# Performance work log

Hardware: AMD Instinct MI355X
Metric: run time of the kernel (lower is better)

The kernel has to match this reference:

```python
import jax, jax.numpy as jnp
import numpy as np

D_MODEL, H, G = 2048, 32, 8
D_K = D_MODEL // H          # 64
GROUP_SIZE = H // G         # 4
B, S = 2, 2048


def setup_inputs() -> dict:
    key = jax.random.key(0)
    ks = jax.random.split(key, 9)
    sd = 1.0 / np.sqrt(D_MODEL)
    x = jax.random.normal(ks[0], (B, S, D_MODEL), dtype=jnp.float32)
    Wq = jax.random.normal(ks[1], (D_MODEL, D_MODEL), dtype=jnp.float32) * sd
    bq = jax.random.normal(ks[2], (D_MODEL,), dtype=jnp.float32) * 0.01
    Wk = jax.random.normal(ks[3], (D_MODEL, G * D_K), dtype=jnp.float32) * sd
    bk = jax.random.normal(ks[4], (G * D_K,), dtype=jnp.float32) * 0.01
    Wv = jax.random.normal(ks[5], (D_MODEL, G * D_K), dtype=jnp.float32) * sd
    bv = jax.random.normal(ks[6], (G * D_K,), dtype=jnp.float32) * 0.01
    Wo = jax.random.normal(ks[7], (D_MODEL, D_MODEL), dtype=jnp.float32) * sd
    bo = jax.random.normal(ks[8], (D_MODEL,), dtype=jnp.float32) * 0.01
    return {"x": x, "Wq": Wq, "bq": bq, "Wk": Wk, "bk": bk,
            "Wv": Wv, "bv": bv, "Wo": Wo, "bo": bo}


def reference(x, Wq, bq, Wk, bk, Wv, bv, Wo, bo):
    Bsz, Sln, _ = x.shape
    # projections
    Q = (x @ Wq + bq).reshape(Bsz, Sln, H, D_K).transpose(0, 2, 1, 3)   # [B,h,S,dk]
    K = (x @ Wk + bk).reshape(Bsz, Sln, G, D_K).transpose(0, 2, 1, 3)   # [B,g,S,dk]
    V = (x @ Wv + bv).reshape(Bsz, Sln, G, D_K).transpose(0, 2, 1, 3)   # [B,g,S,dk]
    # reshape Q into groups: [B, g, group_size, S, dk]; K/V broadcast over group dim
    Qg = Q.reshape(Bsz, G, GROUP_SIZE, Sln, D_K)
    scores = jnp.einsum('bgmqd,bgkd->bgmqk', Qg, K) / jnp.sqrt(jnp.float32(D_K))
    attn = jax.nn.softmax(scores, axis=-1)                              # [B,g,gs,S,S]
    out = jnp.einsum('bgmqk,bgkd->bgmqd', attn, V)                      # [B,g,gs,S,dk]
    out = out.reshape(Bsz, H, Sln, D_K).transpose(0, 2, 1, 3).reshape(Bsz, Sln, D_MODEL)
    return out @ Wo + bo
```

## Files before the change

kernel.cpp:

```cpp
#include <hip/hip_runtime.h>
#include <stdint.h>

#define DMODEL 2048
#define NHEADS 32
#define NGRP 8
#define DKH 64
#define BATCH 2
#define SEQ 2048
#define MTOT (BATCH*SEQ)

typedef unsigned short u16;
typedef __bf16 bf16x8 __attribute__((ext_vector_type(8)));
typedef float f32x4 __attribute__((ext_vector_type(4)));
typedef _Float16 f16x4 __attribute__((ext_vector_type(4)));
typedef _Float16 f16x8 __attribute__((ext_vector_type(8)));
typedef _Float16 f16x2 __attribute__((ext_vector_type(2)));

#define QSCALE 0.18033688011112042f

__device__ __forceinline__ u16 f2bf(float f){
    uint32_t x = __float_as_uint(f);
    x += 0x7FFFu + ((x >> 16) & 1u);
    return (u16)(x >> 16);
}

__device__ __forceinline__ void gld_lds16(const u16* g, u16* l){
    __builtin_amdgcn_global_load_lds(
        (const __attribute__((address_space(1))) uint32_t*)g,
        (__attribute__((address_space(3))) uint32_t*)l, 16, 0, 0);
}


__global__ void cvt_x_kern(const float* __restrict__ x, u16* __restrict__ xb){
    int i = (blockIdx.x * 256 + threadIdx.x) * 4;
    float4 v = *(const float4*)(x + i);
    uint32_t lo = (uint32_t)f2bf(v.x) | ((uint32_t)f2bf(v.y) << 16);
    uint32_t hi = (uint32_t)f2bf(v.z) | ((uint32_t)f2bf(v.w) << 16);
    *(uint2*)(xb + i) = make_uint2(lo, hi);
}

__global__ void cvt_wT_all(const float* __restrict__ Wq, const float* __restrict__ Wk,
                           const float* __restrict__ Wv, const float* __restrict__ Wo,
                           u16* __restrict__ WqT, u16* __restrict__ WkT,
                           u16* __restrict__ WvT, u16* __restrict__ WoT){
    __shared__ float t[32][33];
    int bx = blockIdx.x;
    const float* W; u16* T; int N; int cx;
    if (bx < 64)      { W = Wq; T = WqT; N = 2048; cx = bx; }
    else if (bx < 80) { W = Wk; T = WkT; N = 512;  cx = bx - 64; }
    else if (bx < 96) { W = Wv; T = WvT; N = 512;  cx = bx - 80; }
    else              { W = Wo; T = WoT; N = 2048; cx = bx - 96; }
    int tx = threadIdx.x & 31, ty = threadIdx.x >> 5;
    int n0 = cx * 32, k0 = blockIdx.y * 32;
#pragma unroll
    for (int i = 0; i < 4; i++)
        t[ty*4+i][tx] = W[(size_t)(k0 + ty*4 + i) * N + n0 + tx];
    __syncthreads();
#pragma unroll
    for (int i = 0; i < 4; i++)
        T[(size_t)(n0 + ty*4 + i) * DMODEL + k0 + tx] = f2bf(t[tx][ty*4+i]);
}

template<int EPI>
__global__ __launch_bounds__(256, 2) void gemm_nt(
    const u16* __restrict__ A, const u16* __restrict__ Bt,
    const float* __restrict__ bias0, const float* __restrict__ bias1, const float* __restrict__ bias2,
    void* __restrict__ out0, void* __restrict__ out1, void* __restrict__ out2, int Kn)
{
    __shared__ alignas(16) u16 As[128*32];
    __shared__ alignas(16) u16 Bs[128*32];
    const int tid  = threadIdx.x;
    const int w    = tid >> 6, lane = tid & 63, quad = lane >> 4, l16 = lane & 15;
    const int wr   = w >> 1,  wc   = w & 1;
    const int m0   = blockIdx.x * 128, n0 = blockIdx.y * 128;
    const int arow = lane >> 2, acol = (lane & 3) * 8;

    const u16* ga = A  + (size_t)(m0 + w*32 + arow) * Kn + acol;
    const u16* gb = Bt + (size_t)(n0 + w*32 + arow) * Kn + acol;
    u16* la = As + (w*32) * 32;
    u16* lb = Bs + (w*32) * 32;

    f32x4 acc[4][4] = {};

    for (int k0 = 0; k0 < Kn; k0 += 32){
        __syncthreads();
        gld_lds16(ga + k0,                  la);
        gld_lds16(ga + k0 + (size_t)16*Kn,  la + 16*32);
        gld_lds16(gb + k0,                  lb);
        gld_lds16(gb + k0 + (size_t)16*Kn,  lb + 16*32);
        __syncthreads();
        bf16x8 af[4], bfr[4];
#pragma unroll
        for (int t = 0; t < 4; t++)
            af[t]  = *(const bf16x8*)(As + (wr*64 + t*16 + l16)*32 + quad*8);
#pragma unroll
        for (int t = 0; t < 4; t++)
            bfr[t] = *(const bf16x8*)(Bs + (wc*64 + t*16 + l16)*32 + quad*8);
#pragma unroll
        for (int tm = 0; tm < 4; tm++)
#pragma unroll
            for (int tn = 0; tn < 4; tn++)
                acc[tm][tn] = __builtin_amdgcn_mfma_f32_16x16x32_bf16(af[tm], bfr[tn], acc[tm][tn], 0, 0, 0);
    }

#pragma unroll
    for (int tn = 0; tn < 4; tn++){
        int col = n0 + wc*64 + tn*16 + l16;
        float bv;
        if (EPI == 3) bv = (col < 2048) ? bias0[col] : (col < 2560) ? bias1[col-2048] : bias2[col-2560];
        else          bv = bias0[col];
#pragma unroll
        for (int tm = 0; tm < 4; tm++){
#pragma unroll
            for (int r = 0; r < 4; r++){
                int row = m0 + wr*64 + tm*16 + quad*4 + r;
                float v = acc[tm][tn][r] + bv;
                if (EPI == 3){
                    int b = row >> 11, s = row & (SEQ-1);
                    if (col < 2048){
                        int hh = col >> 6, d = col & 63;
                        ((u16*)out0)[(((size_t)b*NHEADS + hh)*SEQ + s)*DKH + d] = f2bf(v * QSCALE);
                    } else if (col < 2560){
                        int c = col - 2048, gg = c >> 6, d = c & 63;
                        ((u16*)out1)[(((size_t)b*NGRP + gg)*SEQ + s)*DKH + d] = f2bf(v);
                    } else {
                        int c = col - 2560, gg = c >> 6, d = c & 63;
                        int t = s & 31;
                        int pos = (t < 16) ? (((t >> 2) << 3) | (t & 3))
                                           : ((((t & 15) >> 2) << 3) | 4 | (t & 3));
                        int sp = (s & ~31) | pos;
                        ((u16*)out2)[(((size_t)b*NGRP + gg)*DKH + d)*SEQ + sp] =
                            __builtin_bit_cast(u16, (_Float16)v);
                    }
                } else {
                    ((float*)out0)[(size_t)row * DMODEL + col] = v;
                }
            }
        }
    }
}

__global__ __launch_bounds__(256, 4) void flash_kern(
    const u16* __restrict__ Qb, const u16* __restrict__ Kb,
    const u16* __restrict__ Vt, u16* __restrict__ Ob)
{
    __shared__ alignas(16) u16 Ks[2][64*64];
    __shared__ alignas(16) u16 Vs[2][64*64];
    const int tid = threadIdx.x, w = tid >> 6, lane = tid & 63;
    const int quad = lane >> 4, l16 = lane & 15;
    const int q0 = blockIdx.x * 128;
    const int h  = blockIdx.y, b = blockIdx.z, g = h >> 2;

    const u16* Qg = Qb + (((size_t)b*NHEADS + h)*SEQ + q0 + w*32) * DKH;
    const u16* Kg = Kb + ((size_t)b*NGRP + g) * SEQ * DKH;
    const u16* Vg = Vt + ((size_t)b*NGRP + g) * DKH * SEQ;

    const int lr = lane >> 3, lc = lane & 7;
    const int sw = lc ^ lr;
    const u16* gk0 = Kg + (size_t)(w*16 + lr) * DKH + sw*8;
    const u16* gv0 = Vg + (size_t)(w*16 + lr) * SEQ + sw*8;

    bf16x8 aq[2][2];
#pragma unroll
    for (int nt = 0; nt < 2; nt++)
#pragma unroll
        for (int ks = 0; ks < 2; ks++)
            aq[ks][nt] = *(const bf16x8*)(Qg + (nt*16 + l16)*DKH + ks*32 + quad*8);

    float lsum[2] = {};
    f32x4 oa[2][4] = {};

#define STAGE(buf, kt) do{                                                        \
        gld_lds16(gk0 + (size_t)(kt)*64*DKH,           Ks[buf] + (w*16)*64);      \
        gld_lds16(gk0 + (size_t)(kt)*64*DKH + 8*DKH,   Ks[buf] + (w*16+8)*64);    \
        gld_lds16(gv0 + (size_t)(kt)*64,               Vs[buf] + (w*16)*64);      \
        gld_lds16(gv0 + (size_t)(kt)*64 + (size_t)8*SEQ, Vs[buf] + (w*16+8)*64);  \
    }while(0)

#define COMPUTE(buf) do{                                                              \
        _Pragma("unroll")                                                             \
        for (int p = 0; p < 2; p++){                                                  \
            f16x4 pe[2], po[2];                                                       \
            _Pragma("unroll")                                                         \
            for (int hf = 0; hf < 2; hf++){                                           \
                const int kc = p*2 + hf;                                              \
                bf16x8 bk0 = *(const bf16x8*)(Ks[buf] + (kc*16 + l16)*64              \
                                              + ((quad     ^ (l16&7)) * 8));          \
                bf16x8 bk1 = *(const bf16x8*)(Ks[buf] + (kc*16 + l16)*64              \
                                              + (((4+quad) ^ (l16&7)) * 8));          \
                _Pragma("unroll")                                                     \
                for (int nt = 0; nt < 2; nt++){                                       \
                    f32x4 sa = {};                                                    \
                    sa = __builtin_amdgcn_mfma_f32_16x16x32_bf16(bk0, aq[0][nt], sa,0,0,0);\
                    sa = __builtin_amdgcn_mfma_f32_16x16x32_bf16(bk1, aq[1][nt], sa,0,0,0);\
                    float e0 = __builtin_amdgcn_exp2f(sa[0]);                         \
                    float e1 = __builtin_amdgcn_exp2f(sa[1]);                         \
                    float e2 = __builtin_amdgcn_exp2f(sa[2]);                         \
                    float e3 = __builtin_amdgcn_exp2f(sa[3]);                         \
                    lsum[nt] += (e0 + e1) + (e2 + e3);                                \
                    uint2 pk = make_uint2(                                            \
                        __builtin_bit_cast(uint32_t, __builtin_amdgcn_cvt_pkrtz(e0, e1)), \
                        __builtin_bit_cast(uint32_t, __builtin_amdgcn_cvt_pkrtz(e2, e3)));\
                    (hf ? po : pe)[nt] = __builtin_bit_cast(f16x4, pk);               \
                }                                                                     \
            }                                                                         \
            f16x8 pa8[2];                                                             \
            _Pragma("unroll")                                                         \
            for (int nt = 0; nt < 2; nt++)                                            \
                pa8[nt] = __builtin_shufflevector(pe[nt], po[nt], 0,1,2,3,4,5,6,7);   \
            _Pragma("unroll")                                                         \
            for (int dt = 0; dt < 4; dt++){                                           \
                f16x8 bv8 = *(const f16x8*)(Vs[buf] + (dt*16 + l16)*64                \
                             + (((4*p + quad) ^ (l16&7)) * 8));                       \
                _Pragma("unroll")                                                     \
                for (int nt = 0; nt < 2; nt++)                                        \
                    oa[nt][dt] = __builtin_amdgcn_mfma_f32_16x16x32_f16(              \
                        pa8[nt], bv8, oa[nt][dt], 0, 0, 0);                           \
            }                                                                         \
        }                                                                             \
    }while(0)

    STAGE(0, 0);
    __syncthreads();

    for (int kt2 = 0; kt2 < SEQ/128; ++kt2){
        int kt = kt2 * 2;
        STAGE(1, kt + 1);
        COMPUTE(0);
        __syncthreads();
        if (kt2 < SEQ/128 - 1) STAGE(0, kt + 2);
        COMPUTE(1);
        __syncthreads();
    }

#pragma unroll
    for (int nt = 0; nt < 2; nt++){
        float s = lsum[nt];
        s += __shfl_xor(s, 16, 64);
        s += __shfl_xor(s, 32, 64);
        lsum[nt] = 1.0f / s;
    }

#pragma unroll
    for (int nt = 0; nt < 2; nt++)
#pragma unroll
        for (int r = 0; r < 4; r++){
            float inv = __shfl(lsum[nt], quad*4 + r, 64);
            int q = q0 + w*32 + nt*16 + quad*4 + r;
#pragma unroll
            for (int dt = 0; dt < 4; dt++)
                Ob[((size_t)b*SEQ + q)*DMODEL + h*DKH + dt*16 + l16] = f2bf(oa[nt][dt][r] * inv);
        }
#undef STAGE
#undef COMPUTE
}


extern "C" void kernel_launch(void* const* d_in, const int* in_sizes, int n_in,
                              void* d_out, int out_size, void* d_ws, size_t ws_size,
                              hipStream_t stream)
{
    const float* x  = (const float*)d_in[0];
    const float* Wq = (const float*)d_in[1];
    const float* bq = (const float*)d_in[2];
    const float* Wk = (const float*)d_in[3];
    const float* bk = (const float*)d_in[4];
    const float* Wv = (const float*)d_in[5];
    const float* bv = (const float*)d_in[6];
    const float* Wo = (const float*)d_in[7];
    const float* bo = (const float*)d_in[8];

    uint8_t* p = (uint8_t*)d_ws;
    u16* xb  = (u16*)p; p += (size_t)MTOT*DMODEL*2;
    u16* WqT = (u16*)p; p += (size_t)DMODEL*DMODEL*2;
    u16* WkT = (u16*)p; p += (size_t)(NGRP*DKH)*DMODEL*2;
    u16* WvT = (u16*)p; p += (size_t)(NGRP*DKH)*DMODEL*2;
    u16* WoT = (u16*)p; p += (size_t)DMODEL*DMODEL*2;
    u16* Qb  = (u16*)p; p += (size_t)BATCH*NHEADS*SEQ*DKH*2;
    u16* Kb  = (u16*)p; p += (size_t)BATCH*NGRP*SEQ*DKH*2;
    u16* Vtb = (u16*)p; p += (size_t)BATCH*NGRP*DKH*SEQ*2;
    u16* Ob  = (u16*)p; p += (size_t)MTOT*DMODEL*2;

    cvt_x_kern<<<MTOT*DMODEL/1024, 256, 0, stream>>>(x, xb);
    cvt_wT_all<<<dim3(160, 64), 256, 0, stream>>>(Wq, Wk, Wv, Wo, WqT, WkT, WvT, WoT);

    gemm_nt<3><<<dim3(MTOT/128, 3072/128), 256, 0, stream>>>(
        xb, WqT, bq, bk, bv, Qb, Kb, Vtb, DMODEL);

    flash_kern<<<dim3(SEQ/128, NHEADS, BATCH), 256, 0, stream>>>(Qb, Kb, Vtb, Ob);

    gemm_nt<2><<<dim3(MTOT/128, DMODEL/128), 256, 0, stream>>>(
        Ob, WoT, bo, nullptr, nullptr, d_out, nullptr, nullptr, DMODEL);
}
```

Measured before the change: 316.7 us.

## Fuse conversion kernels, remap GEMM blocks per XCD, raise QKV GEMM occupancy

```diff
diff --git a/kernel.cpp b/kernel.cpp
--- a/kernel.cpp
+++ b/kernel.cpp
@@ -14,7 +14,6 @@
 typedef float f32x4 __attribute__((ext_vector_type(4)));
 typedef _Float16 f16x4 __attribute__((ext_vector_type(4)));
 typedef _Float16 f16x8 __attribute__((ext_vector_type(8)));
-typedef _Float16 f16x2 __attribute__((ext_vector_type(2)));
 
 #define QSCALE 0.18033688011112042f
 
@@ -30,28 +29,30 @@
         (__attribute__((address_space(3))) uint32_t*)l, 16, 0, 0);
 }
 
-
-__global__ void cvt_x_kern(const float* __restrict__ x, u16* __restrict__ xb){
-    int i = (blockIdx.x * 256 + threadIdx.x) * 4;
-    float4 v = *(const float4*)(x + i);
-    uint32_t lo = (uint32_t)f2bf(v.x) | ((uint32_t)f2bf(v.y) << 16);
-    uint32_t hi = (uint32_t)f2bf(v.z) | ((uint32_t)f2bf(v.w) << 16);
-    *(uint2*)(xb + i) = make_uint2(lo, hi);
-}
-
-__global__ void cvt_wT_all(const float* __restrict__ Wq, const float* __restrict__ Wk,
-                           const float* __restrict__ Wv, const float* __restrict__ Wo,
-                           u16* __restrict__ WqT, u16* __restrict__ WkT,
-                           u16* __restrict__ WvT, u16* __restrict__ WoT){
+__global__ void cvt_fused(const float* __restrict__ x, u16* __restrict__ xb,
+                          const float* __restrict__ Wq, const float* __restrict__ Wk,
+                          const float* __restrict__ Wv, const float* __restrict__ Wo,
+                          u16* __restrict__ WqT, u16* __restrict__ WkT,
+                          u16* __restrict__ WvT, u16* __restrict__ WoT){
     __shared__ float t[32][33];
-    int bx = blockIdx.x;
+    int bid = blockIdx.x;
+    if (bid < 8192){
+        int i = (bid * 256 + threadIdx.x) * 4;
+        float4 v = *(const float4*)(x + i);
+        uint32_t lo = (uint32_t)f2bf(v.x) | ((uint32_t)f2bf(v.y) << 16);
+        uint32_t hi = (uint32_t)f2bf(v.z) | ((uint32_t)f2bf(v.w) << 16);
+        *(uint2*)(xb + i) = make_uint2(lo, hi);
+        return;
+    }
+    int id = bid - 8192;
+    int bx = id % 160, ky = id / 160;
     const float* W; u16* T; int N; int cx;
     if (bx < 64)      { W = Wq; T = WqT; N = 2048; cx = bx; }
     else if (bx < 80) { W = Wk; T = WkT; N = 512;  cx = bx - 64; }
     else if (bx < 96) { W = Wv; T = WvT; N = 512;  cx = bx - 80; }
     else              { W = Wo; T = WoT; N = 2048; cx = bx - 96; }
     int tx = threadIdx.x & 31, ty = threadIdx.x >> 5;
-    int n0 = cx * 32, k0 = blockIdx.y * 32;
+    int n0 = cx * 32, k0 = ky * 32;
 #pragma unroll
     for (int i = 0; i < 4; i++)
         t[ty*4+i][tx] = W[(size_t)(k0 + ty*4 + i) * N + n0 + tx];
@@ -61,8 +62,8 @@
         T[(size_t)(n0 + ty*4 + i) * DMODEL + k0 + tx] = f2bf(t[tx][ty*4+i]);
 }
 
-template<int EPI>
-__global__ __launch_bounds__(256, 2) void gemm_nt(
+template<int EPI, int MINW>
+__global__ __launch_bounds__(256, MINW) void gemm_nt(
     const u16* __restrict__ A, const u16* __restrict__ Bt,
     const float* __restrict__ bias0, const float* __restrict__ bias1, const float* __restrict__ bias2,
     void* __restrict__ out0, void* __restrict__ out1, void* __restrict__ out2, int Kn)
@@ -72,7 +73,14 @@
     const int tid  = threadIdx.x;
     const int w    = tid >> 6, lane = tid & 63, quad = lane >> 4, l16 = lane & 15;
     const int wr   = w >> 1,  wc   = w & 1;
-    const int m0   = blockIdx.x * 128, n0 = blockIdx.y * 128;
+
+    int bid = blockIdx.y * gridDim.x + blockIdx.x;
+    int nwg = gridDim.x * gridDim.y;
+    int cpx = nwg >> 3;
+    int sbid = (bid & 7) * cpx + (bid >> 3);
+    int bx = sbid % gridDim.x, by = sbid / gridDim.x;
+    const int m0 = bx * 128, n0 = by * 128;
+
     const int arow = lane >> 2, acol = (lane & 3) * 8;
 
     const u16* ga = A  + (size_t)(m0 + w*32 + arow) * Kn + acol;
@@ -281,14 +289,13 @@
     u16* Vtb = (u16*)p; p += (size_t)BATCH*NGRP*DKH*SEQ*2;
     u16* Ob  = (u16*)p; p += (size_t)MTOT*DMODEL*2;
 
-    cvt_x_kern<<<MTOT*DMODEL/1024, 256, 0, stream>>>(x, xb);
-    cvt_wT_all<<<dim3(160, 64), 256, 0, stream>>>(Wq, Wk, Wv, Wo, WqT, WkT, WvT, WoT);
-
-    gemm_nt<3><<<dim3(MTOT/128, 3072/128), 256, 0, stream>>>(
+    cvt_fused<<<18432, 256, 0, stream>>>(x, xb, Wq, Wk, Wv, Wo, WqT, WkT, WvT, WoT);
+
+    gemm_nt<3,3><<<dim3(MTOT/128, 3072/128), 256, 0, stream>>>(
         xb, WqT, bq, bk, bv, Qb, Kb, Vtb, DMODEL);
 
     flash_kern<<<dim3(SEQ/128, NHEADS, BATCH), 256, 0, stream>>>(Qb, Kb, Vtb, Ob);
 
-    gemm_nt<2><<<dim3(MTOT/128, DMODEL/128), 256, 0, stream>>>(
+    gemm_nt<2,2><<<dim3(MTOT/128, DMODEL/128), 256, 0, stream>>>(
         Ob, WoT, bo, nullptr, nullptr, d_out, nullptr, nullptr, DMODEL);
 }
```

After: 329.0 us. 1.04x slower.
